# Kernel optimization log

Measured on AMD Instinct MI355X. Metric: run time of the kernel, lower is better.

## Reference

```python
import jax, jax.numpy as jnp
import numpy as np

K = 15.0          # sigmoid sharpness in get_approxi
THETA2 = 400.0    # gaussian 'theta2' parameter
LOSS_WEIGHT = 1.0


def obb2poly_le90(boxes):
    # boxes [..., 5] = (x, y, w, h, a) -> poly [..., 8]
    x, y, w, h, a = (boxes[..., i] for i in range(5))
    cosa, sina = jnp.cos(a), jnp.sin(a)
    wx, wy = 0.5 * w * cosa, 0.5 * w * sina
    hx, hy = -0.5 * h * sina, 0.5 * h * cosa
    return jnp.stack([
        x - wx - hx, y - wy - hy,
        x + wx - hx, y + wy - hy,
        x + wx + hx, y + wy + hy,
        x - wx + hx, y - wy + hy,
    ], axis=-1)


def setup_inputs() -> dict:
    key = jax.random.key(0)
    k1, k2, k3, k4, k5, k6 = jax.random.split(key, 6)
    N, M = 256, 512

    def make_boxes(k):
        u = jax.random.uniform(k, (N, 5), dtype=jnp.float32)
        cx = 100.0 + 300.0 * u[:, 0]
        cy = 100.0 + 300.0 * u[:, 1]
        w = 20.0 + 100.0 * u[:, 2]
        h = 20.0 + 100.0 * u[:, 3]
        a = (u[:, 4] - 0.5) * (jnp.pi / 2)
        return jnp.stack([cx, cy, w, h, a], axis=-1)

    pred = make_boxes(k1)
    target = make_boxes(k2)
    mask = 512.0 * jax.random.uniform(k3, (N, M, 2), dtype=jnp.float32)
    grad_x = jax.random.normal(k4, (N, M), dtype=jnp.float32)
    grad_y = jax.random.normal(k5, (N, M), dtype=jnp.float32)
    offset = 50.0 * jax.random.uniform(k6, (N, 2), dtype=jnp.float32)
    return {"pred": pred, "target": target, "mask": mask,
            "grad_x": grad_x, "grad_y": grad_y, "offset": offset}


def _my_loss(pred, target, mask, grad_x, grad_y, offset):
    # pred/target [N,5], mask [N,M,2], grad_x/grad_y [N,M], offset [N,2]
    px = pred[:, 0] - offset[:, 0]   # [N]
    py = pred[:, 1] - offset[:, 1]
    pw, ph, pa = pred[:, 2], pred[:, 3], pred[:, 4]
    gx = target[:, 0] - offset[:, 0]
    gy = target[:, 1] - offset[:, 1]
    gw, gh, ga = target[:, 2], target[:, 3], target[:, 4]

    mx, my = mask[..., 0], mask[..., 1]            # [N,M]
    dx = mx - gx[:, None]
    dy = my - gy[:, None]
    d = jnp.sqrt(dx * dx + dy * dy)                # [N,M]
    acos_arg = jnp.clip((gx[:, None] - mx) / d, -1.0, 1.0)
    acosv = jnp.arccos(acos_arg)
    beta = jnp.where(gy[:, None] >= my, ga[:, None] + acosv, ga[:, None] - acosv)

    d_w = jnp.abs(d * jnp.cos(beta))
    d_h = jnp.abs(d * jnp.sin(beta))
    sig = jax.nn.sigmoid
    approxi_1 = (1.0 - sig(K * (d_w - gw[:, None]) / gw[:, None])) * \
                (1.0 - sig(K * (d_h - gh[:, None]) / gh[:, None]))  # [N,M]

    d_w_p = pw[:, None] * d_w / gw[:, None]
    d_h_p = ph[:, None] * d_h / gh[:, None]
    zeros = jnp.zeros_like(d_w_p)
    boxes = jnp.stack([zeros, zeros, 2.0 * d_w_p, 2.0 * d_h_p,
                       jnp.broadcast_to(pa[:, None], d_w_p.shape)], axis=-1)
    pts = obb2poly_le90(boxes)                     # [N,M,8]

    half_pi = jnp.pi / 2
    q2 = (beta > -half_pi) & (beta <= 0.0)
    q3 = (beta > -jnp.pi) & (beta <= -half_pi)
    q4 = (beta > half_pi) & (beta <= jnp.pi)
    # default (q1: 0 < beta <= pi/2) -> corner 0
    gpx = jnp.where(q2, pts[..., 2], jnp.where(q3, pts[..., 4], jnp.where(q4, pts[..., 6], pts[..., 0])))
    gpy = jnp.where(q2, pts[..., 3], jnp.where(q3, pts[..., 5], jnp.where(q4, pts[..., 7], pts[..., 1])))
    guass_x = px[:, None] + gpx                    # [N,M]
    guass_y = py[:, None] + gpy

    # approxi_2[n,i,j] = exp(+||guass_i - mask_j||^2 / (2*theta2^2)) / (2*pi*theta2)
    dgx = guass_x[:, :, None] - mx[:, None, :]
    dgy = guass_y[:, :, None] - my[:, None, :]
    approxi_2 = jnp.exp((dgx * dgx + dgy * dgy) / (2.0 * THETA2 * THETA2)) / (2.0 * jnp.pi * THETA2)

    # w[n,i,j] = gx_i*gx_j + gy_i*gy_j
    w = grad_x[:, :, None] * grad_x[:, None, :] + grad_y[:, :, None] * grad_y[:, None, :]

    loss_per_box = jnp.mean(w * approxi_2 * approxi_1[:, None, :], axis=(1, 2))  # [N]
    return loss_per_box


def reference(pred, target, mask, grad_x, grad_y, offset):
    loss_per_box = _my_loss(pred, target, mask, grad_x, grad_y, offset)
    return LOSS_WEIGHT * jnp.mean(loss_per_box)  # reduction='mean'
```

## Files before the change

### kernel.cpp

```cpp
#include <hip/hip_runtime.h>
#include <math.h>

typedef float v2f __attribute__((ext_vector_type(2)));

#define N_BOX   256
#define M_PTS   512
#define S_SPLIT 8
#define BLK     64
#define R_ROWS  8
#define M2_PER  (M_PTS / S_SPLIT)
#define GRID    (N_BOX * S_SPLIT)

__global__ __launch_bounds__(BLK, 2) void loss_main(
    const float* __restrict__ pred,
    const float* __restrict__ target,
    const float* __restrict__ mask,
    const float* __restrict__ gradx,
    const float* __restrict__ grady,
    const float* __restrict__ offset,
    float* __restrict__ part)
{
    __shared__ float4 sPack[M2_PER];

    const int n = blockIdx.x >> 3;
    const int s = blockIdx.x & 7;
    const int t = threadIdx.x;

    const float offx = offset[n * 2 + 0];
    const float offy = offset[n * 2 + 1];
    const float px = pred[n * 5 + 0] - offx;
    const float py = pred[n * 5 + 1] - offy;
    const float pw = pred[n * 5 + 2];
    const float ph = pred[n * 5 + 3];
    const float pa = pred[n * 5 + 4];
    const float gx = target[n * 5 + 0] - offx;
    const float gy = target[n * 5 + 1] - offy;
    const float gw = target[n * 5 + 2];
    const float gh = target[n * 5 + 3];
    const float ga = target[n * 5 + 4];

    float sinpa, cospa, singa, cosga;
    sincosf(pa, &sinpa, &cospa);
    sincosf(ga, &singa, &cosga);

    const float THETA2   = 400.0f;
    const float LOG2E    = 1.4426950408889634f;
    const float c1       = LOG2E / (2.0f * THETA2 * THETA2);
    const float rs       = sqrtf(c1);
    const float inv_norm = 1.0f / (2.0f * (float)M_PI * THETA2);

    const float pwg = pw / gw, phg = ph / gh;
    const float cwx = pwg * cospa, swx = pwg * sinpa;
    const float chx = phg * cospa, shx = phg * sinpa;
    const float absinga = fabsf(singa);
    const float kA  = 15.0f * LOG2E / gw;
    const float kH  = 15.0f * LOG2E / gh;
    const float kB  = 15.0f * LOG2E;
    const float pxrs = px * rs, pyrs = py * rs;
    const bool  gaPos = (ga > 0.0f), gaNeg = (ga < 0.0f);

    const float2* mask2 = (const float2*)mask;
    const size_t  baseM = (size_t)n * M_PTS;

    v2f Gx[4], Gy[4], gvx2[4], gvy2[4];

#pragma unroll
    for (int r = 0; r < R_ROWS; ++r) {
        const int    m  = t + (r << 6);
        const float2 mp = mask2[baseM + m];
        const float dx = mp.x - gx;
        const float dy = mp.y - gy;
        const float u = singa * dy - cosga * dx;
        const float v = -(cosga * dy + singa * dx);
        const bool sgaOk = gaPos ? (dy <= 0.0f) : (gaNeg ? (dy > 0.0f) : false);
        const bool wrap  = sgaOk && (dx > 0.0f) && (dx * absinga > fabsf(dy) * cosga);
        const float au = fabsf(u), av = fabsf(v);
        const float dws = (wrap || v > 0.0f) ? -au : au;
        const float dhs = (wrap || u > 0.0f) ? -av : av;
        const float gpx = dws * cwx - dhs * shx;
        const float gpy = dws * swx + dhs * chx;
        const float gvx = gradx[baseM + m];
        const float gvy = grady[baseM + m];
        Gx[r >> 1][r & 1]   = fmaf(gpx, rs, pxrs);
        Gy[r >> 1][r & 1]   = fmaf(gpy, rs, pyrs);
        gvx2[r >> 1][r & 1] = gvx;
        gvy2[r >> 1][r & 1] = gvy;
        if (r == s) {
            const float eA = __builtin_amdgcn_exp2f(fmaf(au, kA, -kB));
            const float eB = __builtin_amdgcn_exp2f(fmaf(av, kH, -kB));
            const float B  = inv_norm / ((1.0f + eA) * (1.0f + eB));
            sPack[t] = make_float4(mp.x * rs, mp.y * rs, gvx * B, gvy * B);
        }
    }
    __syncthreads();

    v2f accz[4], accw[4];
#pragma unroll
    for (int q = 0; q < 4; ++q) { accz[q] = (v2f)0.0f; accw[q] = (v2f)0.0f; }

#pragma unroll 4
    for (int m2 = 0; m2 < M2_PER; ++m2) {
        const float4 p = sPack[m2];
#pragma unroll
        for (int q = 0; q < 4; ++q) {
            v2f dgx = Gx[q] - p.x;
            v2f dgy = Gy[q] - p.y;
            v2f sa  = dgx * dgx + dgy * dgy;
            v2f e;
            e.x = __builtin_amdgcn_exp2f(sa.x);
            e.y = __builtin_amdgcn_exp2f(sa.y);
            accz[q] += e * p.z;
            accw[q] += e * p.w;
        }
    }

    v2f tot2 = accz[0] * gvx2[0] + accw[0] * gvy2[0];
    tot2 += accz[1] * gvx2[1] + accw[1] * gvy2[1];
    tot2 += accz[2] * gvx2[2] + accw[2] * gvy2[2];
    tot2 += accz[3] * gvx2[3] + accw[3] * gvy2[3];
    float acc = tot2.x + tot2.y;

#pragma unroll
    for (int off = 32; off > 0; off >>= 1)
        acc += __shfl_down(acc, off, 64);
    if (t == 0) part[blockIdx.x] = acc;
}

__global__ __launch_bounds__(256) void loss_reduce(const float* __restrict__ part,
                                                   float* __restrict__ out)
{
    __shared__ float sW[4];
    const int t = threadIdx.x;
    const float4* p4 = (const float4*)part;
    const float4 a = p4[t];
    const float4 b = p4[t + 256];
    float acc = ((a.x + a.y) + (a.z + a.w)) + ((b.x + b.y) + (b.z + b.w));
#pragma unroll
    for (int off = 32; off > 0; off >>= 1)
        acc += __shfl_down(acc, off, 64);
    if ((t & 63) == 0) sW[t >> 6] = acc;
    __syncthreads();
    if (t == 0) {
        const float scale = 1.0f / ((float)N_BOX * (float)M_PTS * (float)M_PTS);
        out[0] = (sW[0] + sW[1] + sW[2] + sW[3]) * scale;
    }
}

extern "C" void kernel_launch(void* const* d_in, const int* in_sizes, int n_in,
                              void* d_out, int out_size, void* d_ws, size_t ws_size,
                              hipStream_t stream) {
    const float* pred   = (const float*)d_in[0];
    const float* target = (const float*)d_in[1];
    const float* mask   = (const float*)d_in[2];
    const float* gradx  = (const float*)d_in[3];
    const float* grady  = (const float*)d_in[4];
    const float* offset = (const float*)d_in[5];
    float* out  = (float*)d_out;
    float* part = (float*)d_ws;

    hipLaunchKernelGGL(loss_main, dim3(GRID), dim3(BLK), 0, stream,
                       pred, target, mask, gradx, grady, offset, part);
    hipLaunchKernelGGL(loss_reduce, dim3(1), dim3(256), 0, stream, part, out);
}
```

Measured before the change: 82.25 us.

## Split per-point precompute into separate kernel and widen pair-sum blocks

Moves the per-point geometry (gaussian corner positions, sigmoid weights, gradient products) into a dedicated precompute kernel that writes two float4 arrays to workspace. The pair-sum kernel then uses 256-thread blocks, each thread handling 2 rows, reading precomputed data instead of redoing the per-row geometry 8 times per box. This removes the redundant recomputation across the 8 split blocks and raises per-block parallelism. In exchange it adds a kernel launch plus a global-memory round trip for the intermediates, and gives each thread less register-level reuse of each shared-memory load.

```diff
diff --git a/kernel.cpp b/kernel.cpp
--- a/kernel.cpp
+++ b/kernel.cpp
@@ -6,25 +6,23 @@
 #define N_BOX   256
 #define M_PTS   512
 #define S_SPLIT 8
-#define BLK     64
-#define R_ROWS  8
+#define BLK_B   256
 #define M2_PER  (M_PTS / S_SPLIT)
-#define GRID    (N_BOX * S_SPLIT)
+#define GRID_B  (N_BOX * S_SPLIT)
 
-__global__ __launch_bounds__(BLK, 2) void loss_main(
+
+__global__ __launch_bounds__(512) void precompute(
     const float* __restrict__ pred,
     const float* __restrict__ target,
     const float* __restrict__ mask,
     const float* __restrict__ gradx,
     const float* __restrict__ grady,
     const float* __restrict__ offset,
-    float* __restrict__ part)
+    float4* __restrict__ P1,
+    float4* __restrict__ P2)
 {
-    __shared__ float4 sPack[M2_PER];
-
-    const int n = blockIdx.x >> 3;
-    const int s = blockIdx.x & 7;
-    const int t = threadIdx.x;
+    const int n = blockIdx.x;
+    const int m = threadIdx.x;
 
     const float offx = offset[n * 2 + 0];
     const float offy = offset[n * 2 + 1];
@@ -60,70 +58,78 @@
     const bool  gaPos = (ga > 0.0f), gaNeg = (ga < 0.0f);
 
     const float2* mask2 = (const float2*)mask;
-    const size_t  baseM = (size_t)n * M_PTS;
+    const size_t  idx   = (size_t)n * M_PTS + m;
 
-    v2f Gx[4], Gy[4], gvx2[4], gvy2[4];
+    const float2 mp = mask2[idx];
+    const float dx = mp.x - gx;
+    const float dy = mp.y - gy;
+    const float u = singa * dy - cosga * dx;
+    const float v = -(cosga * dy + singa * dx);
+    const bool sgaOk = gaPos ? (dy <= 0.0f) : (gaNeg ? (dy > 0.0f) : false);
+    const bool wrap  = sgaOk && (dx > 0.0f) && (dx * absinga > fabsf(dy) * cosga);
+    const float au = fabsf(u), av = fabsf(v);
+    const float dws = (wrap || v > 0.0f) ? -au : au;
+    const float dhs = (wrap || u > 0.0f) ? -av : av;
+    const float gpx = dws * cwx - dhs * shx;
+    const float gpy = dws * swx + dhs * chx;
+    const float gvx = gradx[idx];
+    const float gvy = grady[idx];
 
-#pragma unroll
-    for (int r = 0; r < R_ROWS; ++r) {
-        const int    m  = t + (r << 6);
-        const float2 mp = mask2[baseM + m];
-        const float dx = mp.x - gx;
-        const float dy = mp.y - gy;
-        const float u = singa * dy - cosga * dx;
-        const float v = -(cosga * dy + singa * dx);
-        const bool sgaOk = gaPos ? (dy <= 0.0f) : (gaNeg ? (dy > 0.0f) : false);
-        const bool wrap  = sgaOk && (dx > 0.0f) && (dx * absinga > fabsf(dy) * cosga);
-        const float au = fabsf(u), av = fabsf(v);
-        const float dws = (wrap || v > 0.0f) ? -au : au;
-        const float dhs = (wrap || u > 0.0f) ? -av : av;
-        const float gpx = dws * cwx - dhs * shx;
-        const float gpy = dws * swx + dhs * chx;
-        const float gvx = gradx[baseM + m];
-        const float gvy = grady[baseM + m];
-        Gx[r >> 1][r & 1]   = fmaf(gpx, rs, pxrs);
-        Gy[r >> 1][r & 1]   = fmaf(gpy, rs, pyrs);
-        gvx2[r >> 1][r & 1] = gvx;
-        gvy2[r >> 1][r & 1] = gvy;
-        if (r == s) {
-            const float eA = __builtin_amdgcn_exp2f(fmaf(au, kA, -kB));
-            const float eB = __builtin_amdgcn_exp2f(fmaf(av, kH, -kB));
-            const float B  = inv_norm / ((1.0f + eA) * (1.0f + eB));
-            sPack[t] = make_float4(mp.x * rs, mp.y * rs, gvx * B, gvy * B);
-        }
-    }
+    const float eA = __builtin_amdgcn_exp2f(fmaf(au, kA, -kB));
+    const float eB = __builtin_amdgcn_exp2f(fmaf(av, kH, -kB));
+    const float B  = inv_norm / ((1.0f + eA) * (1.0f + eB));
+
+    P1[idx] = make_float4(fmaf(gpx, rs, pxrs), fmaf(gpy, rs, pyrs), gvx, gvy);
+    P2[idx] = make_float4(mp.x * rs, mp.y * rs, gvx * B, gvy * B);
+}
+
+__global__ __launch_bounds__(BLK_B, 8) void pair_sum(
+    const float4* __restrict__ P1,
+    const float4* __restrict__ P2,
+    float* __restrict__ part)
+{
+    __shared__ float4 sP[M2_PER];
+    const int n = blockIdx.x >> 3;
+    const int s = blockIdx.x & 7;
+    const int t = threadIdx.x;
+
+    const size_t base = (size_t)n * M_PTS;
+    if (t < M2_PER) sP[t] = P2[base + s * M2_PER + t];
+
+    const float4 g0 = P1[base + t];
+    const float4 g1 = P1[base + t + 256];
     __syncthreads();
 
-    v2f accz[4], accw[4];
-#pragma unroll
-    for (int q = 0; q < 4; ++q) { accz[q] = (v2f)0.0f; accw[q] = (v2f)0.0f; }
+    v2f Gx = {g0.x, g1.x};
+    v2f Gy = {g0.y, g1.y};
+    v2f accz = (v2f)0.0f, accw = (v2f)0.0f;
 
 #pragma unroll 4
     for (int m2 = 0; m2 < M2_PER; ++m2) {
-        const float4 p = sPack[m2];
-#pragma unroll
-        for (int q = 0; q < 4; ++q) {
-            v2f dgx = Gx[q] - p.x;
-            v2f dgy = Gy[q] - p.y;
-            v2f sa  = dgx * dgx + dgy * dgy;
-            v2f e;
-            e.x = __builtin_amdgcn_exp2f(sa.x);
-            e.y = __builtin_amdgcn_exp2f(sa.y);
-            accz[q] += e * p.z;
-            accw[q] += e * p.w;
-        }
+        const float4 p = sP[m2];
+        v2f dgx = Gx - p.x;
+        v2f dgy = Gy - p.y;
+        v2f sa  = dgx * dgx + dgy * dgy;
+        v2f e;
+        e.x = __builtin_amdgcn_exp2f(sa.x);
+        e.y = __builtin_amdgcn_exp2f(sa.y);
+        accz += e * p.z;
+        accw += e * p.w;
     }
 
-    v2f tot2 = accz[0] * gvx2[0] + accw[0] * gvy2[0];
-    tot2 += accz[1] * gvx2[1] + accw[1] * gvy2[1];
-    tot2 += accz[2] * gvx2[2] + accw[2] * gvy2[2];
-    tot2 += accz[3] * gvx2[3] + accw[3] * gvy2[3];
-    float acc = tot2.x + tot2.y;
+    v2f gvx = {g0.z, g1.z};
+    v2f gvy = {g0.w, g1.w};
+    v2f tot = accz * gvx + accw * gvy;
+    float acc = tot.x + tot.y;
 
 #pragma unroll
     for (int off = 32; off > 0; off >>= 1)
         acc += __shfl_down(acc, off, 64);
-    if (t == 0) part[blockIdx.x] = acc;
+
+    __shared__ float sW[4];
+    if ((t & 63) == 0) sW[t >> 6] = acc;
+    __syncthreads();
+    if (t == 0) part[blockIdx.x] = sW[0] + sW[1] + sW[2] + sW[3];
 }
 
 __global__ __launch_bounds__(256) void loss_reduce(const float* __restrict__ part,
@@ -155,10 +161,15 @@
     const float* gradx  = (const float*)d_in[3];
     const float* grady  = (const float*)d_in[4];
     const float* offset = (const float*)d_in[5];
-    float* out  = (float*)d_out;
-    float* part = (float*)d_ws;
+    float* out = (float*)d_out;
 
-    hipLaunchKernelGGL(loss_main, dim3(GRID), dim3(BLK), 0, stream,
-                       pred, target, mask, gradx, grady, offset, part);
+    float4* P1  = (float4*)d_ws;
+    float4* P2  = (float4*)((char*)d_ws + (2u << 20));
+    float*  part = (float*)((char*)d_ws + (4u << 20));
+
+    hipLaunchKernelGGL(precompute, dim3(N_BOX), dim3(M_PTS), 0, stream,
+                       pred, target, mask, gradx, grady, offset, P1, P2);
+    hipLaunchKernelGGL(pair_sum, dim3(GRID_B), dim3(BLK_B), 0, stream,
+                       P1, P2, part);
     hipLaunchKernelGGL(loss_reduce, dim3(1), dim3(256), 0, stream, part, out);
 }
```

After: 84.01 us. 2.1% more time.
